# Performance work log

Hardware: AMD Instinct MI355X
Metric: run time of the kernel (lower is better)

## Reference

```python
import jax, jax.numpy as jnp
import numpy as np

DIM = 1024
HEADS = 16
HEAD_DIM = DIM // HEADS
SCALE = 1.0 / float(np.sqrt(HEAD_DIM))


def complex_linear(x, w_r, w_i, b_r, b_i):
    # x: (..., in, 2) with trailing real/imag channel
    xr, xi = x[..., 0], x[..., 1]
    lin_rr = xr @ w_r.T + b_r
    lin_ii = xi @ w_i.T + b_i
    lin_ri = xr @ w_i.T + b_i
    lin_ir = xi @ w_r.T + b_r
    out_r = lin_rr - lin_ii
    out_i = lin_ri + lin_ir
    return jnp.stack([out_r, out_i], axis=-1)


def setup_inputs() -> dict:
    key = jax.random.key(0)
    ks = jax.random.split(key, 9)
    B, N = 2, 2048
    s_in = 1.0 / np.sqrt(DIM)
    inp = {
        "x": jax.random.normal(ks[0], (B, N, DIM, 2), dtype=jnp.float32),
        "wqkv_r": jax.random.uniform(ks[1], (3 * DIM, DIM), jnp.float32, -s_in, s_in),
        "wqkv_i": jax.random.uniform(ks[2], (3 * DIM, DIM), jnp.float32, -s_in, s_in),
        "bqkv_r": jax.random.uniform(ks[3], (3 * DIM,), jnp.float32, -s_in, s_in),
        "bqkv_i": jax.random.uniform(ks[4], (3 * DIM,), jnp.float32, -s_in, s_in),
        "wo_r": jax.random.uniform(ks[5], (DIM, DIM), jnp.float32, -s_in, s_in),
        "wo_i": jax.random.uniform(ks[6], (DIM, DIM), jnp.float32, -s_in, s_in),
        "bo_r": jax.random.uniform(ks[7], (DIM,), jnp.float32, -s_in, s_in),
        "bo_i": jax.random.uniform(ks[8], (DIM,), jnp.float32, -s_in, s_in),
    }
    return inp


def reference(x, wqkv_r, wqkv_i, bqkv_r, bqkv_i, wo_r, wo_i, bo_r, bo_i):
    B, N, C, _ = x.shape
    qkv = complex_linear(x, wqkv_r, wqkv_i, bqkv_r, bqkv_i)  # (B,N,3C,2)
    q, k, v = jnp.split(qkv, 3, axis=-2)
    q = q.reshape(B, N, HEADS, HEAD_DIM, 2)
    k = k.reshape(B, N, HEADS, HEAD_DIM, 2)
    v = v.reshape(B, N, HEADS, HEAD_DIM, 2)
    # contract over head_dim AND complex channel: Re(q . conj(k))
    attn = jnp.einsum('bnhdc,bmhdc->bhnm', q, k) * SCALE
    attn = jax.nn.softmax(attn, axis=-1)
    out = jnp.einsum('bhnm,bmhdc->bnhdc', attn, v).reshape(B, N, C, 2)
    return complex_linear(out, wo_r, wo_i, bo_r, bo_i)
```

## Files before the change

### kernel.cpp

```cpp
#include <hip/hip_runtime.h>

using f16 = _Float16;
typedef f16 f16x8 __attribute__((ext_vector_type(8)));
typedef f16 f16x4 __attribute__((ext_vector_type(4)));
typedef float f32x4 __attribute__((ext_vector_type(4)));

#define TOKENS 4096
#define KD 2048
#define NQ 6144
#define QKW 4128
#define VTS 2064

__device__ __forceinline__ void gload_lds16(const void* g, void* l) {
  __builtin_amdgcn_global_load_lds(
      (__attribute__((address_space(1))) void*)(unsigned long long)g,
      (__attribute__((address_space(3))) void*)l, 16, 0, 0);
}

__global__ __launch_bounds__(256) void cast_x_kernel(const float* __restrict__ x,
                                                     f16* __restrict__ X, int n) {
  int i = blockIdx.x * 256 + threadIdx.x;
  if (i < n) X[i] = (f16)x[i];
}

__global__ __launch_bounds__(256) void pack_wqkv_kernel(const float* __restrict__ wr,
    const float* __restrict__ wi, const float* __restrict__ br, const float* __restrict__ bi,
    f16* __restrict__ Wp, float* __restrict__ biasq) {
  int idx = blockIdx.x * 256 + threadIdx.x;
  if (idx >= NQ * KD) return;
  int j = idx >> 11;
  int k = idx & 2047;
  int which = j >> 11;
  int rem = j & 2047;
  int h = rem >> 7, t = rem & 127, d = t >> 1, c = t & 1;
  int o = which * 1024 + h * 64 + d;
  int dk = k >> 1, ck = k & 1;
  float wrv = wr[o * 1024 + dk], wiv = wi[o * 1024 + dk];
  float v = (c == 0) ? ((ck == 0) ? wrv : -wiv) : ((ck == 0) ? wiv : wrv);
  Wp[idx] = (f16)v;
  if (k == 0) biasq[j] = (c == 0) ? (br[o] - bi[o]) : (br[o] + bi[o]);
}

__global__ __launch_bounds__(256) void pack_wo_kernel(const float* __restrict__ wr,
    const float* __restrict__ wi, const float* __restrict__ br, const float* __restrict__ bi,
    f16* __restrict__ Wp, float* __restrict__ biaso) {
  int idx = blockIdx.x * 256 + threadIdx.x;
  if (idx >= KD * KD) return;
  int j = idx >> 11, k = idx & 2047;
  int jo = j >> 1, c = j & 1;
  int dk = k >> 1, ck = k & 1;
  float wrv = wr[jo * 1024 + dk], wiv = wi[jo * 1024 + dk];
  float v = (c == 0) ? ((ck == 0) ? wrv : -wiv) : ((ck == 0) ? wiv : wrv);
  Wp[idx] = (f16)v;
  if (k == 0) biaso[j] = (c == 0) ? (br[jo] - bi[jo]) : (br[jo] + bi[jo]);
}

template<bool HALF_OUT>
__global__ __launch_bounds__(256) void gemm_tn(const f16* __restrict__ A,
    const f16* __restrict__ B, const float* __restrict__ bias,
    void* __restrict__ Cout, int ldc, f16* __restrict__ vt) {
  __shared__ f16 ldsA[128 * 32];
  __shared__ f16 ldsB[128 * 32];
  const int tid = threadIdx.x;
  const int wave = tid >> 6, lane = tid & 63;
  const int lo = lane & 15, hi = lane >> 4;
  const int m0 = blockIdx.y * 128, n0 = blockIdx.x * 128;
  const int wm = wave >> 1, wn = wave & 1;

  const int srow = wave * 32 + (lane >> 2);
  const int scol = (lane & 3) * 8;
  const f16* gA0 = A + (size_t)(m0 + srow) * KD + scol;
  const f16* gA1 = gA0 + (size_t)16 * KD;
  const f16* gB0 = B + (size_t)(n0 + srow) * KD + scol;
  const f16* gB1 = gB0 + (size_t)16 * KD;
  f16* lA0 = &ldsA[wave * 1024];
  f16* lA1 = &ldsA[wave * 1024 + 512];
  f16* lB0 = &ldsB[wave * 1024];
  f16* lB1 = &ldsB[wave * 1024 + 512];

  f32x4 acc[4][4] = {};

  for (int kt = 0; kt < KD; kt += 32) {
    gload_lds16(gA0, lA0);
    gload_lds16(gA1, lA1);
    gload_lds16(gB0, lB0);
    gload_lds16(gB1, lB1);
    gA0 += 32; gA1 += 32; gB0 += 32; gB1 += 32;
    __syncthreads();
    f16x8 af[4], bf[4];
    #pragma unroll
    for (int mi = 0; mi < 4; ++mi)
      af[mi] = *(const f16x8*)&ldsA[(wm * 64 + mi * 16 + lo) * 32 + hi * 8];
    #pragma unroll
    for (int ni = 0; ni < 4; ++ni)
      bf[ni] = *(const f16x8*)&ldsB[(wn * 64 + ni * 16 + lo) * 32 + hi * 8];
    #pragma unroll
    for (int mi = 0; mi < 4; ++mi)
      #pragma unroll
      for (int ni = 0; ni < 4; ++ni)
        acc[mi][ni] = __builtin_amdgcn_mfma_f32_16x16x32_f16(af[mi], bf[ni], acc[mi][ni], 0, 0, 0);
    __syncthreads();
  }

  #pragma unroll
  for (int mi = 0; mi < 4; ++mi) {
    #pragma unroll
    for (int ni = 0; ni < 4; ++ni) {
      const int colbase = n0 + wn * 64 + ni * 16;
      const int col = colbase + lo;
      const float bv = bias[col];
      const int rowb = m0 + wm * 64 + mi * 16 + hi * 4;
      if (vt != nullptr && colbase >= 4096) {
        const int dcol = col - 4096;
        const int hh = dcol >> 7, dd = dcol & 127;
        const int bb = rowb >> 11, tok = rowb & 2047;
        f16x4 pk;
        #pragma unroll
        for (int r = 0; r < 4; ++r) pk[r] = (f16)(acc[mi][ni][r] + bv);
        *(f16x4*)(vt + ((size_t)(bb * 16 + hh) * 128 + dd) * VTS + tok) = pk;
      } else {
        #pragma unroll
        for (int r = 0; r < 4; ++r) {
          const float v = acc[mi][ni][r] + bv;
          if (HALF_OUT) ((f16*)Cout)[(size_t)(rowb + r) * ldc + col] = (f16)v;
          else          ((float*)Cout)[(size_t)(rowb + r) * ldc + col] = v;
        }
      }
    }
  }
}

__global__ __launch_bounds__(256) void attn_kernel(const f16* __restrict__ qk,
                                                   const f16* __restrict__ vt,
                                                   f16* __restrict__ outp) {
  __shared__ __align__(16) f16 lds[2][8192];
  const int tid = threadIdx.x;
  const int wave = tid >> 6, lane = tid & 63;
  const int lo = lane & 15, hi = lane >> 4;

  const int flat = blockIdx.x;
  const int nf = (flat & 7) * 64 + (flat >> 3);
  const int by = nf >> 4, bx = nf & 15;
  const int b = by >> 4, h = by & 15;
  const int q0 = bx * 128 + wave * 32;

  const f16* Qb = qk + (size_t)b * 2048 * QKW + h * 128;
  const f16* Kb = Qb + 2048;
  const f16* Vtb = vt + (size_t)(b * 16 + h) * 128 * VTS;

  f16x8 qf[2][4];
  #pragma unroll
  for (int qb = 0; qb < 2; ++qb)
    #pragma unroll
    for (int c = 0; c < 4; ++c) {
      qf[qb][c] = *(const f16x8*)(Qb + (size_t)(q0 + qb * 16 + lo) * QKW + c * 32 + hi * 8);
      qf[qb][c] *= (f16)0.125f;
    }

  f32x4 o[2][8];
  #pragma unroll
  for (int qb = 0; qb < 2; ++qb)
    #pragma unroll
    for (int dc = 0; dc < 8; ++dc) o[qb][dc] = (f32x4){0.f, 0.f, 0.f, 0.f};
  float m_run[2] = {-INFINITY, -INFINITY};
  float l_run[2] = {0.f, 0.f};

  const int cl0 = wave * 64 + lane;

  auto STAGE = [&](int buf, int t) {
    #pragma unroll
    for (int rnd = 0; rnd < 2; ++rnd) {
      const int cl = rnd * 256 + cl0;
      const int row = cl >> 4;
      const int gch = (cl & 15) ^ (row & 7);
      gload_lds16(Kb + (size_t)(t + row) * QKW + gch * 8,
                  &lds[buf][(size_t)(rnd * 256 + wave * 64) * 8]);
    }
    #pragma unroll
    for (int rnd = 0; rnd < 2; ++rnd) {
      const int cl = rnd * 256 + cl0;
      const int d = cl >> 2;
      const int gch = (cl & 3) ^ ((d >> 1) & 3);
      gload_lds16(Vtb + (size_t)d * VTS + t + gch * 8,
                  &lds[buf][4096 + (size_t)(rnd * 256 + wave * 64) * 8]);
    }
  };

  STAGE(0, 0);
  int cur = 0;

  for (int it = 0; it < 64; ++it) {
    __syncthreads();
    if (it + 1 < 64) STAGE(cur ^ 1, (it + 1) * 32);

    const f16* ldsK = lds[cur];
    const f16* ldsV = lds[cur] + 4096;

    f16x8 kf[2][4];
    #pragma unroll
    for (int tt = 0; tt < 2; ++tt)
      #pragma unroll
      for (int c = 0; c < 4; ++c) {
        const int row = tt * 16 + lo;
        const int ch = (c * 4 + hi) ^ (row & 7);
        kf[tt][c] = *(const f16x8*)&ldsK[row * 128 + ch * 8];
      }

    f16x4 pf[2][2];
    #pragma unroll
    for (int qb = 0; qb < 2; ++qb) {
      f32x4 s0 = {0.f, 0.f, 0.f, 0.f}, s1 = {0.f, 0.f, 0.f, 0.f};
      #pragma unroll
      for (int c = 0; c < 4; ++c) {
        s0 = __builtin_amdgcn_mfma_f32_16x16x32_f16(kf[0][c], qf[qb][c], s0, 0, 0, 0);
        s1 = __builtin_amdgcn_mfma_f32_16x16x32_f16(kf[1][c], qf[qb][c], s1, 0, 0, 0);
      }

      float pm = fmaxf(fmaxf(fmaxf(s0[0], s0[1]), fmaxf(s0[2], s0[3])),
                       fmaxf(fmaxf(s1[0], s1[1]), fmaxf(s1[2], s1[3])));
      pm = fmaxf(pm, __shfl_xor(pm, 16));
      pm = fmaxf(pm, __shfl_xor(pm, 32));

      if (!__all(pm - m_run[qb] <= 8.f)) {
        const float corr = __expf(m_run[qb] - pm);
        m_run[qb] = pm;
        float co[4];
        #pragma unroll
        for (int r = 0; r < 4; ++r) co[r] = __shfl(corr, hi * 4 + r);
        #pragma unroll
        for (int dc = 0; dc < 8; ++dc)
          #pragma unroll
          for (int r = 0; r < 4; ++r) o[qb][dc][r] *= co[r];
        l_run[qb] *= corr;
      }

      float psum = 0.f;
      #pragma unroll
      for (int r = 0; r < 4; ++r) {
        const float p0 = __expf(s0[r] - m_run[qb]);
        const float p1 = __expf(s1[r] - m_run[qb]);
        psum += p0 + p1;
        pf[qb][0][r] = (f16)p0;
        pf[qb][1][r] = (f16)p1;
      }
      psum += __shfl_xor(psum, 16);
      psum += __shfl_xor(psum, 32);
      l_run[qb] += psum;
    }

    #pragma unroll
    for (int dc = 0; dc < 8; ++dc) {
      const int d = dc * 16 + lo;
      f16x4 vf[2];
      #pragma unroll
      for (int tt = 0; tt < 2; ++tt) {
        const int ch = (tt * 2 + (hi >> 1)) ^ ((d >> 1) & 3);
        vf[tt] = *(const f16x4*)&ldsV[d * 32 + ch * 8 + (hi & 1) * 4];
      }
      o[0][dc] = __builtin_amdgcn_mfma_f32_16x16x16f16(pf[0][0], vf[0], o[0][dc], 0, 0, 0);
      o[0][dc] = __builtin_amdgcn_mfma_f32_16x16x16f16(pf[0][1], vf[1], o[0][dc], 0, 0, 0);
      o[1][dc] = __builtin_amdgcn_mfma_f32_16x16x16f16(pf[1][0], vf[0], o[1][dc], 0, 0, 0);
      o[1][dc] = __builtin_amdgcn_mfma_f32_16x16x16f16(pf[1][1], vf[1], o[1][dc], 0, 0, 0);
    }

    cur ^= 1;
  }

  #pragma unroll
  for (int qb = 0; qb < 2; ++qb) {
    float inv[4];
    #pragma unroll
    for (int r = 0; r < 4; ++r) inv[r] = 1.f / __shfl(l_run[qb], hi * 4 + r);
    const int tok0 = b * 2048 + q0 + qb * 16;
    #pragma unroll
    for (int dc = 0; dc < 8; ++dc)
      #pragma unroll
      for (int r = 0; r < 4; ++r)
        outp[(size_t)(tok0 + hi * 4 + r) * KD + h * 128 + dc * 16 + lo] =
            (f16)(o[qb][dc][r] * inv[r]);
  }
}

extern "C" void kernel_launch(void* const* d_in, const int* in_sizes, int n_in,
                              void* d_out, int out_size, void* d_ws, size_t ws_size,
                              hipStream_t stream) {
  const float* x      = (const float*)d_in[0];
  const float* wqkv_r = (const float*)d_in[1];
  const float* wqkv_i = (const float*)d_in[2];
  const float* bqkv_r = (const float*)d_in[3];
  const float* bqkv_i = (const float*)d_in[4];
  const float* wo_r   = (const float*)d_in[5];
  const float* wo_i   = (const float*)d_in[6];
  const float* bo_r   = (const float*)d_in[7];
  const float* bo_i   = (const float*)d_in[8];
  float* out = (float*)d_out;
  char* ws = (char*)d_ws;

  f16*   Wqkv_p = (f16*)(ws + 0);
  f16*   Wo_p   = (f16*)(ws + 25165824);
  float* biasq  = (float*)(ws + 33554432);
  float* biaso  = (float*)(ws + 33579008);
  f16*   qkQK   = (f16*)(ws + 33587200);
  f16*   Vt     = (f16*)(ws + 67403776);
  f16*   Xh     = (f16*)(ws + 84312064);
  f16*   attn16 = Xh;

  cast_x_kernel<<<(TOKENS * KD) / 256, 256, 0, stream>>>(x, Xh, TOKENS * KD);
  pack_wqkv_kernel<<<(NQ * KD) / 256, 256, 0, stream>>>(wqkv_r, wqkv_i, bqkv_r, bqkv_i,
                                                        Wqkv_p, biasq);
  pack_wo_kernel<<<(KD * KD) / 256, 256, 0, stream>>>(wo_r, wo_i, bo_r, bo_i, Wo_p, biaso);

  gemm_tn<true><<<dim3(NQ / 128, TOKENS / 128), 256, 0, stream>>>(
      Xh, Wqkv_p, biasq, (void*)qkQK, QKW, Vt);
  attn_kernel<<<512, 256, 0, stream>>>(qkQK, Vt, attn16);
  gemm_tn<false><<<dim3(KD / 128, TOKENS / 128), 256, 0, stream>>>(
      attn16, Wo_p, biaso, (void*)out, KD, nullptr);
}
```

Measured before the change: 333.4 us.

## Replace QKV GEMM with 256x256-tile, 8-wave, 8-phase pipelined MFMA kernel

```diff
diff --git a/kernel.cpp b/kernel.cpp
--- a/kernel.cpp
+++ b/kernel.cpp
@@ -10,6 +10,9 @@
 #define NQ 6144
 #define QKW 4128
 #define VTS 2064
+
+#define BAR()   asm volatile("s_barrier" ::: "memory")
+#define LGKM0() asm volatile("s_waitcnt lgkmcnt(0)" ::: "memory")
 
 __device__ __forceinline__ void gload_lds16(const void* g, void* l) {
   __builtin_amdgcn_global_load_lds(
@@ -55,10 +58,130 @@
   if (k == 0) biaso[j] = (c == 0) ? (br[jo] - bi[jo]) : (br[jo] + bi[jo]);
 }
 
-template<bool HALF_OUT>
-__global__ __launch_bounds__(256) void gemm_tn(const f16* __restrict__ A,
+__global__ __launch_bounds__(512, 2) void gemm1_8ph(const f16* __restrict__ A,
     const f16* __restrict__ B, const float* __restrict__ bias,
-    void* __restrict__ Cout, int ldc, f16* __restrict__ vt) {
+    f16* __restrict__ qkout, f16* __restrict__ vt) {
+  __shared__ __align__(16) f16 ldsA[2][2][128 * 64];
+  __shared__ __align__(16) f16 ldsB[2][2][128 * 64];
+
+  const int tid = threadIdx.x;
+  const int wave = tid >> 6, lane = tid & 63;
+  const int lo = lane & 15, hi = lane >> 4;
+  const int wm = wave >> 2, wn = wave & 3;
+
+  const int bid = blockIdx.x;
+  const int wg = (bid & 7) * 48 + (bid >> 3);
+  const int tn = wg >> 4, tm = wg & 15;
+  const int m0 = tm * 256, n0 = tn * 256;
+
+  auto stageA = [&](int slot, int half, int u) {
+    const f16* g = A + (size_t)(m0 + half * 128) * KD + u * 64;
+    #pragma unroll
+    for (int is = 0; is < 2; ++is) {
+      const int L = is * 512 + tid;
+      const int row = L >> 3, cp = L & 7;
+      gload_lds16(g + (size_t)row * KD + ((cp ^ (row & 7)) * 8),
+                  &ldsA[slot][half][(is * 512 + wave * 64) * 8]);
+    }
+  };
+  auto stageB = [&](int slot, int half, int u) {
+    const f16* g = B + (size_t)(n0 + half * 128) * KD + u * 64;
+    #pragma unroll
+    for (int is = 0; is < 2; ++is) {
+      const int L = is * 512 + tid;
+      const int row = L >> 3, cp = L & 7;
+      gload_lds16(g + (size_t)row * KD + ((cp ^ (row & 7)) * 8),
+                  &ldsB[slot][half][(is * 512 + wave * 64) * 8]);
+    }
+  };
+  auto readA4 = [&](f16x8* dst, int slot, int mi0, int kk) {
+    #pragma unroll
+    for (int i = 0; i < 4; ++i) {
+      const int row = (mi0 + i) * 16 + lo;
+      const int ch = (kk * 4 + hi) ^ (row & 7);
+      dst[i] = *(const f16x8*)&ldsA[slot][wm][row * 64 + ch * 8];
+    }
+  };
+  auto readB4 = [&](f16x8* dst, int slot, int kk) {
+    #pragma unroll
+    for (int i = 0; i < 4; ++i) {
+      const int row = (wn & 1) * 64 + i * 16 + lo;
+      const int ch = (kk * 4 + hi) ^ (row & 7);
+      dst[i] = *(const f16x8*)&ldsB[slot][wn >> 1][row * 64 + ch * 8];
+    }
+  };
+
+  f32x4 acc[8][4] = {};
+  auto mfma16 = [&](int mh, const f16x8* av, const f16x8* bv) {
+    #pragma unroll
+    for (int mi = 0; mi < 4; ++mi)
+      #pragma unroll
+      for (int ni = 0; ni < 4; ++ni)
+        acc[mh * 4 + mi][ni] = __builtin_amdgcn_mfma_f32_16x16x32_f16(
+            av[mi], bv[ni], acc[mh * 4 + mi][ni], 0, 0, 0);
+  };
+
+  stageA(0, 0, 0); stageA(0, 1, 0);
+  stageB(0, 0, 0); stageB(0, 1, 0);
+  stageB(1, 0, 1); stageB(1, 1, 1);
+  asm volatile("s_waitcnt vmcnt(4)" ::: "memory");
+  BAR();
+
+  const int NT = KD / 64;
+  f16x8 a[4], b0[4], b1[4];
+  for (int u = 0; u < NT; ++u) {
+    const int s = u & 1;
+    readA4(a, s, 0, 0); readB4(b0, s, 0);
+    if (u + 1 < NT) stageA(s ^ 1, 0, u + 1);
+    BAR(); LGKM0();
+    __builtin_amdgcn_s_setprio(1); mfma16(0, a, b0); __builtin_amdgcn_s_setprio(0);
+    BAR();
+    readA4(a, s, 4, 0); readB4(b1, s, 1);
+    if (u + 1 < NT) stageA(s ^ 1, 1, u + 1);
+    BAR(); LGKM0();
+    __builtin_amdgcn_s_setprio(1); mfma16(1, a, b0); __builtin_amdgcn_s_setprio(0);
+    BAR();
+    readA4(a, s, 0, 1);
+    if (u + 2 < NT) stageB(s, 0, u + 2);
+    BAR(); LGKM0();
+    __builtin_amdgcn_s_setprio(1); mfma16(0, a, b1); __builtin_amdgcn_s_setprio(0);
+    BAR();
+    readA4(a, s, 4, 1);
+    if (u + 2 < NT) stageB(s, 1, u + 2);
+    if (u < NT - 2) { asm volatile("s_waitcnt vmcnt(4)" ::: "memory"); }
+    else           { asm volatile("s_waitcnt vmcnt(0)" ::: "memory"); }
+    BAR(); LGKM0();
+    __builtin_amdgcn_s_setprio(1); mfma16(1, a, b1); __builtin_amdgcn_s_setprio(0);
+    BAR();
+  }
+
+  #pragma unroll
+  for (int mi = 0; mi < 8; ++mi) {
+    #pragma unroll
+    for (int ni = 0; ni < 4; ++ni) {
+      const int col = n0 + wn * 64 + ni * 16 + lo;
+      const float bv = bias[col];
+      const int rowb = m0 + wm * 128 + mi * 16 + hi * 4;
+      if (tn >= 16) {
+        const int dcol = col - 4096;
+        const int hh = dcol >> 7, dd = dcol & 127;
+        const int bb = rowb >> 11, tok = rowb & 2047;
+        f16x4 pk;
+        #pragma unroll
+        for (int r = 0; r < 4; ++r) pk[r] = (f16)(acc[mi][ni][r] + bv);
+        *(f16x4*)(vt + ((size_t)(bb * 16 + hh) * 128 + dd) * VTS + tok) = pk;
+      } else {
+        #pragma unroll
+        for (int r = 0; r < 4; ++r)
+          qkout[(size_t)(rowb + r) * QKW + col] = (f16)(acc[mi][ni][r] + bv);
+      }
+    }
+  }
+}
+
+__global__ __launch_bounds__(256) void gemm_tn_f32(const f16* __restrict__ A,
+    const f16* __restrict__ B, const float* __restrict__ bias,
+    float* __restrict__ Cout, int ldc) {
   __shared__ f16 ldsA[128 * 32];
   __shared__ f16 ldsB[128 * 32];
   const int tid = threadIdx.x;
@@ -106,26 +229,12 @@
   for (int mi = 0; mi < 4; ++mi) {
     #pragma unroll
     for (int ni = 0; ni < 4; ++ni) {
-      const int colbase = n0 + wn * 64 + ni * 16;
-      const int col = colbase + lo;
+      const int col = n0 + wn * 64 + ni * 16 + lo;
       const float bv = bias[col];
       const int rowb = m0 + wm * 64 + mi * 16 + hi * 4;
-      if (vt != nullptr && colbase >= 4096) {
-        const int dcol = col - 4096;
-        const int hh = dcol >> 7, dd = dcol & 127;
-        const int bb = rowb >> 11, tok = rowb & 2047;
-        f16x4 pk;
-        #pragma unroll
-        for (int r = 0; r < 4; ++r) pk[r] = (f16)(acc[mi][ni][r] + bv);
-        *(f16x4*)(vt + ((size_t)(bb * 16 + hh) * 128 + dd) * VTS + tok) = pk;
-      } else {
-        #pragma unroll
-        for (int r = 0; r < 4; ++r) {
-          const float v = acc[mi][ni][r] + bv;
-          if (HALF_OUT) ((f16*)Cout)[(size_t)(rowb + r) * ldc + col] = (f16)v;
-          else          ((float*)Cout)[(size_t)(rowb + r) * ldc + col] = v;
-        }
-      }
+      #pragma unroll
+      for (int r = 0; r < 4; ++r)
+        Cout[(size_t)(rowb + r) * ldc + col] = acc[mi][ni][r] + bv;
     }
   }
 }
@@ -310,9 +419,8 @@
                                                         Wqkv_p, biasq);
   pack_wo_kernel<<<(KD * KD) / 256, 256, 0, stream>>>(wo_r, wo_i, bo_r, bo_i, Wo_p, biaso);
 
-  gemm_tn<true><<<dim3(NQ / 128, TOKENS / 128), 256, 0, stream>>>(
-      Xh, Wqkv_p, biasq, (void*)qkQK, QKW, Vt);
+  gemm1_8ph<<<384, 512, 0, stream>>>(Xh, Wqkv_p, biasq, qkQK, Vt);
   attn_kernel<<<512, 256, 0, stream>>>(qkQK, Vt, attn16);
-  gemm_tn<false><<<dim3(KD / 128, TOKENS / 128), 256, 0, stream>>>(
-      attn16, Wo_p, biaso, (void*)out, KD, nullptr);
-}
+  gemm_tn_f32<<<dim3(KD / 128, TOKENS / 128), 256, 0, stream>>>(
+      attn16, Wo_p, biaso, out, KD);
+}
```

Result: slower. 355.0 us (+6.5%).

## Vectorize cast/pack kernels and rework GEMM with K64 swizzled LDS tiles

Applied to the files above, without the earlier changes.

```diff
diff --git a/kernel.cpp b/kernel.cpp
--- a/kernel.cpp
+++ b/kernel.cpp
@@ -18,88 +18,127 @@
 }
 
 __global__ __launch_bounds__(256) void cast_x_kernel(const float* __restrict__ x,
-                                                     f16* __restrict__ X, int n) {
+                                                     f16* __restrict__ X, int n8) {
   int i = blockIdx.x * 256 + threadIdx.x;
-  if (i < n) X[i] = (f16)x[i];
+  if (i >= n8) return;
+  const float4* p = (const float4*)x + (size_t)i * 2;
+  float4 a = p[0], b = p[1];
+  f16x8 v = {(f16)a.x, (f16)a.y, (f16)a.z, (f16)a.w,
+             (f16)b.x, (f16)b.y, (f16)b.z, (f16)b.w};
+  *(f16x8*)(X + (size_t)i * 8) = v;
 }
 
 __global__ __launch_bounds__(256) void pack_wqkv_kernel(const float* __restrict__ wr,
     const float* __restrict__ wi, const float* __restrict__ br, const float* __restrict__ bi,
     f16* __restrict__ Wp, float* __restrict__ biasq) {
   int idx = blockIdx.x * 256 + threadIdx.x;
-  if (idx >= NQ * KD) return;
-  int j = idx >> 11;
-  int k = idx & 2047;
-  int which = j >> 11;
-  int rem = j & 2047;
+  if (idx >= NQ * 256) return;
+  int j = idx >> 8, kc = idx & 255;
+  int which = j >> 11, rem = j & 2047;
   int h = rem >> 7, t = rem & 127, d = t >> 1, c = t & 1;
   int o = which * 1024 + h * 64 + d;
-  int dk = k >> 1, ck = k & 1;
-  float wrv = wr[o * 1024 + dk], wiv = wi[o * 1024 + dk];
-  float v = (c == 0) ? ((ck == 0) ? wrv : -wiv) : ((ck == 0) ? wiv : wrv);
-  Wp[idx] = (f16)v;
-  if (k == 0) biasq[j] = (c == 0) ? (br[o] - bi[o]) : (br[o] + bi[o]);
+  const float4 wr4 = *(const float4*)(wr + (size_t)o * 1024 + kc * 4);
+  const float4 wi4 = *(const float4*)(wi + (size_t)o * 1024 + kc * 4);
+  f16x8 v;
+  const float wrs[4] = {wr4.x, wr4.y, wr4.z, wr4.w};
+  const float wis[4] = {wi4.x, wi4.y, wi4.z, wi4.w};
+  #pragma unroll
+  for (int tt = 0; tt < 4; ++tt) {
+    v[2 * tt]     = (f16)((c == 0) ? wrs[tt] : wis[tt]);
+    v[2 * tt + 1] = (f16)((c == 0) ? -wis[tt] : wrs[tt]);
+  }
+  *(f16x8*)(Wp + (size_t)j * KD + kc * 8) = v;
+  if (kc == 0) biasq[j] = (c == 0) ? (br[o] - bi[o]) : (br[o] + bi[o]);
 }
 
 __global__ __launch_bounds__(256) void pack_wo_kernel(const float* __restrict__ wr,
     const float* __restrict__ wi, const float* __restrict__ br, const float* __restrict__ bi,
     f16* __restrict__ Wp, float* __restrict__ biaso) {
   int idx = blockIdx.x * 256 + threadIdx.x;
-  if (idx >= KD * KD) return;
-  int j = idx >> 11, k = idx & 2047;
+  if (idx >= KD * 256) return;
+  int j = idx >> 8, kc = idx & 255;
   int jo = j >> 1, c = j & 1;
-  int dk = k >> 1, ck = k & 1;
-  float wrv = wr[jo * 1024 + dk], wiv = wi[jo * 1024 + dk];
-  float v = (c == 0) ? ((ck == 0) ? wrv : -wiv) : ((ck == 0) ? wiv : wrv);
-  Wp[idx] = (f16)v;
-  if (k == 0) biaso[j] = (c == 0) ? (br[jo] - bi[jo]) : (br[jo] + bi[jo]);
-}
-
-template<bool HALF_OUT>
-__global__ __launch_bounds__(256) void gemm_tn(const f16* __restrict__ A,
+  const float4 wr4 = *(const float4*)(wr + (size_t)jo * 1024 + kc * 4);
+  const float4 wi4 = *(const float4*)(wi + (size_t)jo * 1024 + kc * 4);
+  f16x8 v;
+  const float wrs[4] = {wr4.x, wr4.y, wr4.z, wr4.w};
+  const float wis[4] = {wi4.x, wi4.y, wi4.z, wi4.w};
+  #pragma unroll
+  for (int tt = 0; tt < 4; ++tt) {
+    v[2 * tt]     = (f16)((c == 0) ? wrs[tt] : wis[tt]);
+    v[2 * tt + 1] = (f16)((c == 0) ? -wis[tt] : wrs[tt]);
+  }
+  *(f16x8*)(Wp + (size_t)j * KD + kc * 8) = v;
+  if (kc == 0) biaso[j] = (c == 0) ? (br[jo] - bi[jo]) : (br[jo] + bi[jo]);
+}
+
+template<bool QKV, int NTN>
+__global__ __launch_bounds__(256, 3) void gemm_v5(const f16* __restrict__ A,
     const f16* __restrict__ B, const float* __restrict__ bias,
-    void* __restrict__ Cout, int ldc, f16* __restrict__ vt) {
-  __shared__ f16 ldsA[128 * 32];
-  __shared__ f16 ldsB[128 * 32];
+    f16* __restrict__ qkout, f16* __restrict__ vt, float* __restrict__ fout) {
+  __shared__ __align__(16) f16 lA[128 * 64];
+  __shared__ __align__(16) f16 lB[128 * 64];
+
   const int tid = threadIdx.x;
   const int wave = tid >> 6, lane = tid & 63;
   const int lo = lane & 15, hi = lane >> 4;
-  const int m0 = blockIdx.y * 128, n0 = blockIdx.x * 128;
   const int wm = wave >> 1, wn = wave & 1;
 
-  const int srow = wave * 32 + (lane >> 2);
-  const int scol = (lane & 3) * 8;
-  const f16* gA0 = A + (size_t)(m0 + srow) * KD + scol;
-  const f16* gA1 = gA0 + (size_t)16 * KD;
-  const f16* gB0 = B + (size_t)(n0 + srow) * KD + scol;
-  const f16* gB1 = gB0 + (size_t)16 * KD;
-  f16* lA0 = &ldsA[wave * 1024];
-  f16* lA1 = &ldsA[wave * 1024 + 512];
-  f16* lB0 = &ldsB[wave * 1024];
-  f16* lB1 = &ldsB[wave * 1024 + 512];
+  const int nwg = gridDim.x, cpx = nwg / 8;
+  const int bid = blockIdx.x;
+  const int wg = (bid & 7) * cpx + (bid >> 3);
+  const int tm = wg / NTN, tn = wg % NTN;
+  const int m0 = tm * 128, n0 = tn * 128;
+
+  const f16* gA = A + (size_t)m0 * KD;
+  const f16* gB = B + (size_t)n0 * KD;
+
+  auto stage = [&](f16* ldsX, const f16* g) {
+    #pragma unroll
+    for (int is = 0; is < 4; ++is) {
+      const int L = is * 256 + tid;
+      const int row = L >> 3, cp = L & 7;
+      gload_lds16(g + (size_t)row * KD + ((cp ^ (row & 7)) * 8),
+                  ldsX + (size_t)(is * 256 + wave * 64) * 8);
+    }
+  };
+  auto readA = [&](f16x8* dst, int kk) {
+    #pragma unroll
+    for (int i = 0; i < 4; ++i) {
+      const int row = wm * 64 + i * 16 + lo;
+      const int ch = (kk * 4 + hi) ^ (row & 7);
+      dst[i] = *(const f16x8*)&lA[row * 64 + ch * 8];
+    }
+  };
+  auto readB = [&](f16x8* dst, int kk) {
+    #pragma unroll
+    for (int i = 0; i < 4; ++i) {
+      const int row = wn * 64 + i * 16 + lo;
+      const int ch = (kk * 4 + hi) ^ (row & 7);
+      dst[i] = *(const f16x8*)&lB[row * 64 + ch * 8];
+    }
+  };
 
   f32x4 acc[4][4] = {};
 
-  for (int kt = 0; kt < KD; kt += 32) {
-    gload_lds16(gA0, lA0);
-    gload_lds16(gA1, lA1);
-    gload_lds16(gB0, lB0);
-    gload_lds16(gB1, lB1);
-    gA0 += 32; gA1 += 32; gB0 += 32; gB1 += 32;
+  for (int kt = 0; kt < KD; kt += 64) {
     __syncthreads();
-    f16x8 af[4], bf[4];
+    stage(lA, gA + kt);
+    stage(lB, gB + kt);
+    __syncthreads();
+    f16x8 a[4], b[4];
+    readA(a, 0); readB(b, 0);
     #pragma unroll
     for (int mi = 0; mi < 4; ++mi)
-      af[mi] = *(const f16x8*)&ldsA[(wm * 64 + mi * 16 + lo) * 32 + hi * 8];
-    #pragma unroll
-    for (int ni = 0; ni < 4; ++ni)
-      bf[ni] = *(const f16x8*)&ldsB[(wn * 64 + ni * 16 + lo) * 32 + hi * 8];
+      #pragma unroll
+      for (int ni = 0; ni < 4; ++ni)
+        acc[mi][ni] = __builtin_amdgcn_mfma_f32_16x16x32_f16(a[mi], b[ni], acc[mi][ni], 0, 0, 0);
+    readA(a, 1); readB(b, 1);
     #pragma unroll
     for (int mi = 0; mi < 4; ++mi)
       #pragma unroll
       for (int ni = 0; ni < 4; ++ni)
-        acc[mi][ni] = __builtin_amdgcn_mfma_f32_16x16x32_f16(af[mi], bf[ni], acc[mi][ni], 0, 0, 0);
-    __syncthreads();
+        acc[mi][ni] = __builtin_amdgcn_mfma_f32_16x16x32_f16(a[mi], b[ni], acc[mi][ni], 0, 0, 0);
   }
 
   #pragma unroll
@@ -110,7 +149,7 @@
       const int col = colbase + lo;
       const float bv = bias[col];
       const int rowb = m0 + wm * 64 + mi * 16 + hi * 4;
-      if (vt != nullptr && colbase >= 4096) {
+      if (QKV && colbase >= 4096) {
         const int dcol = col - 4096;
         const int hh = dcol >> 7, dd = dcol & 127;
         const int bb = rowb >> 11, tok = rowb & 2047;
@@ -118,13 +157,14 @@
         #pragma unroll
         for (int r = 0; r < 4; ++r) pk[r] = (f16)(acc[mi][ni][r] + bv);
         *(f16x4*)(vt + ((size_t)(bb * 16 + hh) * 128 + dd) * VTS + tok) = pk;
+      } else if (QKV) {
+        #pragma unroll
+        for (int r = 0; r < 4; ++r)
+          qkout[(size_t)(rowb + r) * QKW + col] = (f16)(acc[mi][ni][r] + bv);
       } else {
         #pragma unroll
-        for (int r = 0; r < 4; ++r) {
-          const float v = acc[mi][ni][r] + bv;
-          if (HALF_OUT) ((f16*)Cout)[(size_t)(rowb + r) * ldc + col] = (f16)v;
-          else          ((float*)Cout)[(size_t)(rowb + r) * ldc + col] = v;
-        }
+        for (int r = 0; r < 4; ++r)
+          fout[(size_t)(rowb + r) * KD + col] = acc[mi][ni][r] + bv;
       }
     }
   }
@@ -305,14 +345,12 @@
   f16*   Xh     = (f16*)(ws + 84312064);
   f16*   attn16 = Xh;
 
-  cast_x_kernel<<<(TOKENS * KD) / 256, 256, 0, stream>>>(x, Xh, TOKENS * KD);
-  pack_wqkv_kernel<<<(NQ * KD) / 256, 256, 0, stream>>>(wqkv_r, wqkv_i, bqkv_r, bqkv_i,
-                                                        Wqkv_p, biasq);
-  pack_wo_kernel<<<(KD * KD) / 256, 256, 0, stream>>>(wo_r, wo_i, bo_r, bo_i, Wo_p, biaso);
-
-  gemm_tn<true><<<dim3(NQ / 128, TOKENS / 128), 256, 0, stream>>>(
-      Xh, Wqkv_p, biasq, (void*)qkQK, QKW, Vt);
+  cast_x_kernel<<<(TOKENS * KD / 8) / 256, 256, 0, stream>>>(x, Xh, TOKENS * KD / 8);
+  pack_wqkv_kernel<<<(NQ * 256) / 256, 256, 0, stream>>>(wqkv_r, wqkv_i, bqkv_r, bqkv_i,
+                                                         Wqkv_p, biasq);
+  pack_wo_kernel<<<(KD * 256) / 256, 256, 0, stream>>>(wo_r, wo_i, bo_r, bo_i, Wo_p, biaso);
+
+  gemm_v5<true, 48><<<1536, 256, 0, stream>>>(Xh, Wqkv_p, biasq, qkQK, Vt, nullptr);
   attn_kernel<<<512, 256, 0, stream>>>(qkQK, Vt, attn16);
-  gemm_tn<false><<<dim3(KD / 128, TOKENS / 128), 256, 0, stream>>>(
-      attn16, Wo_p, biaso, (void*)out, KD, nullptr);
-}
+  gemm_v5<false, 16><<<512, 256, 0, stream>>>(attn16, Wo_p, biaso, nullptr, nullptr, out);
+}
```

New measurement: 317.7 us. 1.05x faster.
